# Kernel optimization log

Measured on AMD Instinct MI355X. Metric: run time of the kernel, lower is better.

## Reference

```python
import jax, jax.numpy as jnp
import numpy as np

EMBED_DIM = 1024
NUM_HEADS = 16
HEAD_DIM = EMBED_DIM // NUM_HEADS


def setup_inputs() -> dict:
    key = jax.random.key(0)
    k1, k2, k3, k4 = jax.random.split(key, 4)
    B, N, D = 4, 2048, EMBED_DIM
    x = jax.random.normal(k1, (B, N, D), dtype=jnp.float32)
    # torch nn.Linear layout: weight [out_features, in_features]
    w_qkv = jax.random.normal(k2, (3 * D, D), dtype=jnp.float32) * (1.0 / np.sqrt(D))
    w_out = jax.random.normal(k3, (D, D), dtype=jnp.float32) * (1.0 / np.sqrt(D))
    b_out = jax.random.normal(k4, (D,), dtype=jnp.float32) * 0.01
    return {"x": x, "w_qkv": w_qkv, "w_out": w_out, "b_out": b_out}


def reference(x, w_qkv, w_out, b_out):
    B, N, D = x.shape
    H, Hd = NUM_HEADS, HEAD_DIM
    qkv = (x @ w_qkv.T).reshape(B, N, 3, H, Hd)
    q, k, v = qkv[:, :, 0], qkv[:, :, 1], qkv[:, :, 2]  # [B,N,H,Hd]
    # NOTE: contracts over BOTH heads and head_dim -> single shared [B,N,N] map
    scores = jnp.einsum('bnhd,bmhd->bnm', q, k) / np.sqrt(Hd).astype(np.float32)
    attn = jax.nn.softmax(scores, axis=-1)
    out = jnp.einsum('bnm,bmhd->bnhd', attn, v).reshape(B, N, D)
    return out @ w_out.T + b_out
```

## Files before the change

kernel.cpp:

```cpp
#include <hip/hip_runtime.h>


typedef __bf16 bf16;
typedef __attribute__((ext_vector_type(8))) __bf16 bf16x8;
typedef __attribute__((ext_vector_type(4))) __bf16 bf16x4;
typedef __attribute__((ext_vector_type(16))) float f32x16;

#define BATCH 4
#define NTOK  2048
#define DIM   1024
#define MROWS (BATCH * NTOK)
#define QKVC  (3 * DIM)

__device__ __forceinline__ void async16(const bf16* g, bf16* l) {
  __builtin_amdgcn_global_load_lds(
      (const __attribute__((address_space(1))) void*)g,
      (__attribute__((address_space(3))) void*)l, 16, 0, 0);
}

__device__ __forceinline__ void cvt4(const float* in, bf16* out, int i4) {
  float4 f = *(const float4*)(in + i4 * 4);
  bf16x4 o;
  o.x = (bf16)f.x; o.y = (bf16)f.y; o.z = (bf16)f.z; o.w = (bf16)f.w;
  *(bf16x4*)(out + i4 * 4) = o;
}

__global__ void prep(const float* __restrict__ x, const float* __restrict__ wqkv,
                     const float* __restrict__ wout,
                     bf16* __restrict__ Xbf, bf16* __restrict__ Wqkvb,
                     bf16* __restrict__ Woutb, float* __restrict__ L) {
  const int nx = MROWS * DIM / 4, nq = QKVC * DIM / 4, nw = DIM * DIM / 4;
  const int nl = BATCH * NTOK / 4;
  int i = blockIdx.x * blockDim.x + threadIdx.x;
  if (i < nx) cvt4(x, Xbf, i);
  else if (i < nx + nq) cvt4(wqkv, Wqkvb, i - nx);
  else if (i < nx + nq + nw) cvt4(wout, Woutb, i - nx - nq);
  else if (i < nx + nq + nw + nl) {
    float4 z = {0.f, 0.f, 0.f, 0.f};
    *(float4*)(L + (i - nx - nq - nw) * 4) = z;
  }
}

struct GemmCore {
  const bf16 *ga[4], *gb[4];
  int sIdx[4];
  int wm, wn, l31, half;
};

__device__ __forceinline__ GemmCore gemm_setup(const bf16* A, const bf16* Bm,
                                               int lda, int ldb,
                                               long rowA, long rowB) {
  GemmCore g;
  const int tid = threadIdx.x;
  const int wave = tid >> 6, lane = tid & 63;
  g.wm = (wave >> 1) << 6;
  g.wn = (wave & 1) << 6;
  g.l31 = lane & 31;
  g.half = lane >> 5;
  const int srow = tid >> 3;
  const int sc   = tid & 7;
  const int scol = (sc ^ (srow & 7)) << 3;
#pragma unroll
  for (int seg = 0; seg < 4; ++seg) {
    g.ga[seg] = A  + (rowA + srow + 32 * seg) * (long)lda + scol;
    g.gb[seg] = Bm + (rowB + srow + 32 * seg) * (long)ldb + scol;
    g.sIdx[seg] = (srow + 32 * seg) * 64 + sc * 8;
  }
  return g;
}

__device__ __forceinline__ void gemm_kloop(const GemmCore& g, int K,
                                           bf16* As, bf16* Bs, f32x16 acc[2][2]) {
  const int sw = g.l31 & 7;
  for (int kt = 0; kt < K; kt += 64) {
#pragma unroll
    for (int seg = 0; seg < 4; ++seg) {
      async16(g.ga[seg] + kt, As + g.sIdx[seg]);
      async16(g.gb[seg] + kt, Bs + g.sIdx[seg]);
    }
    __syncthreads();

    bf16x8 af[2][4], bfm[2][4];
#pragma unroll
    for (int ti = 0; ti < 2; ++ti)
#pragma unroll
      for (int s = 0; s < 4; ++s)
        af[ti][s] = *(const bf16x8*)&As[(g.wm + ti * 32 + g.l31) * 64 + ((s * 2 + g.half) ^ sw) * 8];
#pragma unroll
    for (int tj = 0; tj < 2; ++tj)
#pragma unroll
      for (int s = 0; s < 4; ++s)
        bfm[tj][s] = *(const bf16x8*)&Bs[(g.wn + tj * 32 + g.l31) * 64 + ((s * 2 + g.half) ^ sw) * 8];

#pragma unroll
    for (int s = 0; s < 4; ++s)
#pragma unroll
      for (int ti = 0; ti < 2; ++ti)
#pragma unroll
        for (int tj = 0; tj < 2; ++tj)
          acc[ti][tj] = __builtin_amdgcn_mfma_f32_32x32x16_bf16(
              af[ti][s], bfm[tj][s], acc[ti][tj], 0, 0, 0);

    __syncthreads();
  }
}

template <int MODE>
__launch_bounds__(256)
__global__ void gemm_bt(const bf16* __restrict__ Aroot, const bf16* __restrict__ Broot,
                        void* __restrict__ Croot, const float* __restrict__ bias,
                        const float* __restrict__ Lroot,
                        int K, int lda, int ldb, int ldc,
                        long strideA, long strideB, long strideC) {
  const bf16* A  = Aroot + (long)blockIdx.z * strideA;
  const bf16* Bm = Broot + (long)blockIdx.z * strideB;
  __shared__ alignas(16) bf16 As[128 * 64];
  __shared__ alignas(16) bf16 Bs[128 * 64];

  const long rowA = (long)blockIdx.y * 128;
  const long rowB = (long)blockIdx.x * 128;
  GemmCore g = gemm_setup(A, Bm, lda, ldb, rowA, rowB);

  f32x16 acc[2][2] = {};
  gemm_kloop(g, K, As, Bs, acc);

  if constexpr (MODE == 0) {
    bf16* C = (bf16*)Croot + (long)blockIdx.z * strideC;
#pragma unroll
    for (int ti = 0; ti < 2; ++ti)
#pragma unroll
      for (int tj = 0; tj < 2; ++tj) {
        const long col = rowB + g.wn + tj * 32 + g.l31;
#pragma unroll
        for (int r = 0; r < 16; ++r) {
          const long row = rowA + g.wm + ti * 32 + (r & 3) + 8 * (r >> 2) + 4 * g.half;
          C[row * (long)ldc + col] = (bf16)acc[ti][tj][r];
        }
      }
  } else {
    float* C = (float*)Croot + (long)blockIdx.z * strideC;
    const float* L = Lroot + (long)blockIdx.z * NTOK;
#pragma unroll
    for (int ti = 0; ti < 2; ++ti) {
#pragma unroll
      for (int r = 0; r < 16; ++r) {
        const long row = rowA + g.wm + ti * 32 + (r & 3) + 8 * (r >> 2) + 4 * g.half;
        const float inv = 1.0f / L[row];
#pragma unroll
        for (int tj = 0; tj < 2; ++tj) {
          const long col = rowB + g.wn + tj * 32 + g.l31;
          C[row * (long)ldc + col] = acc[ti][tj][r] * inv + bias[col];
        }
      }
    }
  }
}

__launch_bounds__(256)
__global__ void gemm_sv(const bf16* __restrict__ QKV, const bf16* __restrict__ Wout,
                        bf16* __restrict__ E, bf16* __restrict__ Vpp,
                        float* __restrict__ Lroot) {
  __shared__ alignas(16) bf16 As[128 * 64];
  __shared__ alignas(16) bf16 Bs[128 * 64];

  const int z = blockIdx.z;
  if (z < 4) {
    const bf16* A  = QKV + (long)z * NTOK * QKVC;
    const bf16* Bm = A + DIM;
    const long rowA = (long)blockIdx.y * 128;
    const long rowB = (long)blockIdx.x * 128;
    GemmCore g = gemm_setup(A, Bm, QKVC, QKVC, rowA, rowB);
    f32x16 acc[2][2] = {};
    gemm_kloop(g, DIM, As, Bs, acc);

    bf16* C = E + (long)z * NTOK * NTOK;
    float* L = Lroot + (long)z * NTOK;
#pragma unroll
    for (int ti = 0; ti < 2; ++ti) {
#pragma unroll
      for (int r = 0; r < 16; ++r) {
        const long row = rowA + g.wm + ti * 32 + (r & 3) + 8 * (r >> 2) + 4 * g.half;
        float psum = 0.f;
#pragma unroll
        for (int tj = 0; tj < 2; ++tj) {
          const long col = rowB + g.wn + tj * 32 + g.l31;
          float e = __expf(acc[ti][tj][r] * 0.125f);
          bf16 eb = (bf16)e;
          C[row * (long)NTOK + col] = eb;
          psum += (float)eb;
        }
#pragma unroll
        for (int off = 16; off >= 1; off >>= 1) psum += __shfl_xor(psum, off, 64);
        if (g.l31 == 0) atomicAdd(&L[row], psum);
      }
    }
  } else {
    if (blockIdx.y >= 8) return;
    const int b = z - 4;
    const bf16* Bm = QKV + (long)b * NTOK * QKVC + 2 * DIM;
    const long rowA = (long)blockIdx.y * 128;
    const long rowB = (long)blockIdx.x * 128;
    GemmCore g = gemm_setup(Wout, Bm, DIM, QKVC, rowA, rowB);
    f32x16 acc[2][2] = {};
    gemm_kloop(g, DIM, As, Bs, acc);

    bf16* C = Vpp + (long)b * DIM * NTOK;
#pragma unroll
    for (int ti = 0; ti < 2; ++ti)
#pragma unroll
      for (int tj = 0; tj < 2; ++tj) {
        const long col = rowB + g.wn + tj * 32 + g.l31;
#pragma unroll
        for (int r = 0; r < 16; ++r) {
          const long row = rowA + g.wm + ti * 32 + (r & 3) + 8 * (r >> 2) + 4 * g.half;
          C[row * (long)NTOK + col] = (bf16)acc[ti][tj][r];
        }
      }
  }
}

extern "C" void kernel_launch(void* const* d_in, const int* in_sizes, int n_in,
                              void* d_out, int out_size, void* d_ws, size_t ws_size,
                              hipStream_t stream) {
  const float* x      = (const float*)d_in[0];
  const float* w_qkv  = (const float*)d_in[1];
  const float* w_out  = (const float*)d_in[2];
  const float* b_out  = (const float*)d_in[3];
  float* out = (float*)d_out;

  char* w = (char*)d_ws;
  bf16*  Xbf   = (bf16*)(w);
  bf16*  Wqkvb = (bf16*)(w + 16777216);
  bf16*  Woutb = (bf16*)(w + 23068672);
  bf16*  QKV   = (bf16*)(w + 25165824);
  bf16*  E     = (bf16*)(w + 75497472);
  bf16*  Vpp   = (bf16*)(w + 109051904);
  float* L     = (float*)(w + 125829120);

  {
    const int n4 = MROWS * DIM / 4 + QKVC * DIM / 4 + DIM * DIM / 4 + BATCH * NTOK / 4;
    prep<<<(n4 + 255) / 256, 256, 0, stream>>>(x, w_qkv, w_out, Xbf, Wqkvb, Woutb, L);
  }

  gemm_bt<0><<<dim3(QKVC / 128, MROWS / 128, 1), 256, 0, stream>>>(
      Xbf, Wqkvb, QKV, nullptr, nullptr, DIM, DIM, DIM, QKVC, 0, 0, 0);

  gemm_sv<<<dim3(NTOK / 128, NTOK / 128, 2 * BATCH), 256, 0, stream>>>(
      QKV, Woutb, E, Vpp, L);

  gemm_bt<2><<<dim3(DIM / 128, NTOK / 128, BATCH), 256, 0, stream>>>(
      E, Vpp, out, b_out, L, NTOK, NTOK, NTOK, DIM,
      (long)NTOK * NTOK, (long)DIM * NTOK, (long)NTOK * DIM);
}
```

Baseline: 271.1 us.

## Use 256x256 double-buffered pipelined GEMM for QKV and score/V' projections

Replaces the 128x128 single-buffered GEMM used for the QKV projection and the fused scores/Vout stage with a 256x256-tile, 512-thread kernel. It uses 128KB of dynamic LDS and double-buffers K-tiles so async global-to-LDS loads overlap the MFMA work, with fine-grained vmcnt waits, barriers and setprio. Larger tiles raise arithmetic intensity and cut global traffic. In exchange, fewer blocks give coarser occupancy and wave quantization, and the dynamic shared memory size may need an explicit attribute to launch.

```diff
diff --git a/kernel.cpp b/kernel.cpp
--- a/kernel.cpp
+++ b/kernel.cpp
@@ -11,6 +11,7 @@
 #define DIM   1024
 #define MROWS (BATCH * NTOK)
 #define QKVC  (3 * DIM)
+#define KT256 16
 
 __device__ __forceinline__ void async16(const bf16* g, bf16* l) {
   __builtin_amdgcn_global_load_lds(
@@ -41,6 +42,180 @@
   }
 }
 
+
+template <bool MORE>
+__device__ __forceinline__ void g256_iter(
+    const bf16* Ac, const bf16* Bc, bf16* An, bf16* Bn, int kn,
+    const bf16* gA0, const bf16* gA1, const bf16* gB0, const bf16* gB1,
+    int dst, const int rA[4], const int rB[2], int f, int half,
+    f32x16 acc[4][2]) {
+#pragma unroll
+  for (int p = 0; p < 4; ++p) {
+    const int c = (p & 1) * 2 + half;
+    const int co = ((c ^ f) & 3) * 8 + (p >> 1) * 8192;
+    bf16x8 av[4], bv[2];
+#pragma unroll
+    for (int ti = 0; ti < 4; ++ti) av[ti] = *(const bf16x8*)&Ac[rA[ti] + co];
+#pragma unroll
+    for (int tj = 0; tj < 2; ++tj) bv[tj] = *(const bf16x8*)&Bc[rB[tj] + co];
+    if (MORE) {
+      if (p == 0)      { async16(gA0 + kn,      An + dst);         async16(gA1 + kn,      An + 4096  + dst); }
+      else if (p == 1) { async16(gB0 + kn,      Bn + dst);         async16(gB1 + kn,      Bn + 4096  + dst); }
+      else if (p == 2) { async16(gA0 + kn + 32, An + 8192 + dst);  async16(gA1 + kn + 32, An + 12288 + dst); }
+      else             { async16(gB0 + kn + 32, Bn + 8192 + dst);  async16(gB1 + kn + 32, Bn + 12288 + dst); }
+    }
+    if (p & 1) {
+      if (MORE) asm volatile("s_waitcnt vmcnt(4)" ::: "memory");
+      else      asm volatile("s_waitcnt vmcnt(0)" ::: "memory");
+    }
+    __builtin_amdgcn_sched_barrier(0);
+    __builtin_amdgcn_s_barrier();
+    __builtin_amdgcn_sched_barrier(0);
+    asm volatile("s_waitcnt lgkmcnt(0)" ::: "memory");
+    __builtin_amdgcn_sched_barrier(0);
+    __builtin_amdgcn_s_setprio(1);
+#pragma unroll
+    for (int ti = 0; ti < 4; ++ti)
+#pragma unroll
+      for (int tj = 0; tj < 2; ++tj)
+        acc[ti][tj] = __builtin_amdgcn_mfma_f32_32x32x16_bf16(
+            av[ti], bv[tj], acc[ti][tj], 0, 0, 0);
+    __builtin_amdgcn_s_setprio(0);
+    __builtin_amdgcn_sched_barrier(0);
+    __builtin_amdgcn_s_barrier();
+    __builtin_amdgcn_sched_barrier(0);
+  }
+}
+
+__device__ __forceinline__ void gemm256(const bf16* __restrict__ A,
+                                        const bf16* __restrict__ Bm,
+                                        int lda, int ldb, long rowA, long rowB,
+                                        bf16* sm, int l31, int half, int wr, int wc,
+                                        f32x16 acc[4][2]) {
+  const int tid = threadIdx.x;
+  const int sr = tid >> 2, sq = tid & 3;
+  const int sf = (sr >> 1) & 3;
+  const int scol = (sq ^ sf) * 8;
+  const bf16* gA0 = A  + (rowA + sr) * (long)lda + scol;
+  const bf16* gA1 = A  + (rowA + sr + 128) * (long)lda + scol;
+  const bf16* gB0 = Bm + (rowB + sr) * (long)ldb + scol;
+  const bf16* gB1 = Bm + (rowB + sr + 128) * (long)ldb + scol;
+
+  bf16* Ab0 = sm;
+  bf16* Ab1 = sm + 16384;
+  bf16* Bb0 = sm + 32768;
+  bf16* Bb1 = sm + 49152;
+  const int dst = tid * 8;
+
+  int rA[4], rB[2];
+#pragma unroll
+  for (int ti = 0; ti < 4; ++ti) rA[ti] = (wr * 128 + ti * 32 + l31) * 32;
+#pragma unroll
+  for (int tj = 0; tj < 2; ++tj) rB[tj] = (wc * 64 + tj * 32 + l31) * 32;
+  const int f = (l31 >> 1) & 3;
+
+  async16(gA0, Ab0 + dst);            async16(gA1, Ab0 + 4096 + dst);
+  async16(gB0, Bb0 + dst);            async16(gB1, Bb0 + 4096 + dst);
+  async16(gA0 + 32, Ab0 + 8192 + dst); async16(gA1 + 32, Ab0 + 12288 + dst);
+  async16(gB0 + 32, Bb0 + 8192 + dst); async16(gB1 + 32, Bb0 + 12288 + dst);
+  asm volatile("s_waitcnt vmcnt(4)" ::: "memory");
+  __builtin_amdgcn_sched_barrier(0);
+  __builtin_amdgcn_s_barrier();
+  __builtin_amdgcn_sched_barrier(0);
+
+#pragma unroll 1
+  for (int t2 = 0; t2 < 7; ++t2) {
+    g256_iter<true >(Ab0, Bb0, Ab1, Bb1, (2 * t2 + 1) * 64, gA0, gA1, gB0, gB1, dst, rA, rB, f, half, acc);
+    g256_iter<true >(Ab1, Bb1, Ab0, Bb0, (2 * t2 + 2) * 64, gA0, gA1, gB0, gB1, dst, rA, rB, f, half, acc);
+  }
+  g256_iter<true >(Ab0, Bb0, Ab1, Bb1, 15 * 64, gA0, gA1, gB0, gB1, dst, rA, rB, f, half, acc);
+  g256_iter<false>(Ab1, Bb1, Ab0, Bb0, 0,       gA0, gA1, gB0, gB1, dst, rA, rB, f, half, acc);
+}
+
+__launch_bounds__(512, 2)
+__global__ void gemm256_qkv(const bf16* __restrict__ Xb, const bf16* __restrict__ Wq,
+                            bf16* __restrict__ QKV) {
+  extern __shared__ bf16 sm[];
+  const int tid = threadIdx.x, wave = tid >> 6, lane = tid & 63;
+  const int wr = wave >> 2, wc = wave & 3, l31 = lane & 31, half = lane >> 5;
+  const long rowA = (long)blockIdx.y * 256;
+  const long rowB = (long)blockIdx.x * 256;
+  f32x16 acc[4][2] = {};
+  gemm256(Xb, Wq, DIM, DIM, rowA, rowB, sm, l31, half, wr, wc, acc);
+#pragma unroll
+  for (int ti = 0; ti < 4; ++ti)
+#pragma unroll
+    for (int tj = 0; tj < 2; ++tj) {
+      const long col = rowB + wc * 64 + tj * 32 + l31;
+#pragma unroll
+      for (int r = 0; r < 16; ++r) {
+        const long row = rowA + wr * 128 + ti * 32 + (r & 3) + 8 * (r >> 2) + 4 * half;
+        QKV[row * (long)QKVC + col] = (bf16)acc[ti][tj][r];
+      }
+    }
+}
+
+__launch_bounds__(512, 2)
+__global__ void gemm256_sv(const bf16* __restrict__ QKV, const bf16* __restrict__ Wout,
+                           bf16* __restrict__ E, bf16* __restrict__ Vpp,
+                           float* __restrict__ Lroot) {
+  extern __shared__ bf16 sm[];
+  const int tid = threadIdx.x, wave = tid >> 6, lane = tid & 63;
+  const int wr = wave >> 2, wc = wave & 3, l31 = lane & 31, half = lane >> 5;
+  const int z = blockIdx.z;
+  if (z < 4) {
+    const bf16* A  = QKV + (long)z * NTOK * QKVC;
+    const bf16* Bm = A + DIM;
+    const long rowA = (long)blockIdx.y * 256;
+    const long rowB = (long)blockIdx.x * 256;
+    f32x16 acc[4][2] = {};
+    gemm256(A, Bm, QKVC, QKVC, rowA, rowB, sm, l31, half, wr, wc, acc);
+
+    bf16* C = E + (long)z * NTOK * NTOK;
+    float* L = Lroot + (long)z * NTOK;
+#pragma unroll
+    for (int ti = 0; ti < 4; ++ti) {
+#pragma unroll
+      for (int r = 0; r < 16; ++r) {
+        const long row = rowA + wr * 128 + ti * 32 + (r & 3) + 8 * (r >> 2) + 4 * half;
+        float psum = 0.f;
+#pragma unroll
+        for (int tj = 0; tj < 2; ++tj) {
+          const long col = rowB + wc * 64 + tj * 32 + l31;
+          float e = __expf(acc[ti][tj][r] * 0.125f);
+          bf16 eb = (bf16)e;
+          C[row * (long)NTOK + col] = eb;
+          psum += (float)eb;
+        }
+#pragma unroll
+        for (int off = 16; off >= 1; off >>= 1) psum += __shfl_xor(psum, off, 64);
+        if (l31 == 0) atomicAdd(&L[row], psum);
+      }
+    }
+  } else {
+    if (blockIdx.y >= 4) return;
+    const int b = z - 4;
+    const bf16* Bm = QKV + (long)b * NTOK * QKVC + 2 * DIM;
+    const long rowA = (long)blockIdx.y * 256;
+    const long rowB = (long)blockIdx.x * 256;
+    f32x16 acc[4][2] = {};
+    gemm256(Wout, Bm, DIM, QKVC, rowA, rowB, sm, l31, half, wr, wc, acc);
+
+    bf16* C = Vpp + (long)b * DIM * NTOK;
+#pragma unroll
+    for (int ti = 0; ti < 4; ++ti)
+#pragma unroll
+      for (int tj = 0; tj < 2; ++tj) {
+        const long col = rowB + wc * 64 + tj * 32 + l31;
+#pragma unroll
+        for (int r = 0; r < 16; ++r) {
+          const long row = rowA + wr * 128 + ti * 32 + (r & 3) + 8 * (r >> 2) + 4 * half;
+          C[row * (long)NTOK + col] = (bf16)acc[ti][tj][r];
+        }
+      }
+  }
+}
+
 struct GemmCore {
   const bf16 *ga[4], *gb[4];
   int sIdx[4];
@@ -156,69 +331,6 @@
   }
 }
 
-__launch_bounds__(256)
-__global__ void gemm_sv(const bf16* __restrict__ QKV, const bf16* __restrict__ Wout,
-                        bf16* __restrict__ E, bf16* __restrict__ Vpp,
-                        float* __restrict__ Lroot) {
-  __shared__ alignas(16) bf16 As[128 * 64];
-  __shared__ alignas(16) bf16 Bs[128 * 64];
-
-  const int z = blockIdx.z;
-  if (z < 4) {
-    const bf16* A  = QKV + (long)z * NTOK * QKVC;
-    const bf16* Bm = A + DIM;
-    const long rowA = (long)blockIdx.y * 128;
-    const long rowB = (long)blockIdx.x * 128;
-    GemmCore g = gemm_setup(A, Bm, QKVC, QKVC, rowA, rowB);
-    f32x16 acc[2][2] = {};
-    gemm_kloop(g, DIM, As, Bs, acc);
-
-    bf16* C = E + (long)z * NTOK * NTOK;
-    float* L = Lroot + (long)z * NTOK;
-#pragma unroll
-    for (int ti = 0; ti < 2; ++ti) {
-#pragma unroll
-      for (int r = 0; r < 16; ++r) {
-        const long row = rowA + g.wm + ti * 32 + (r & 3) + 8 * (r >> 2) + 4 * g.half;
-        float psum = 0.f;
-#pragma unroll
-        for (int tj = 0; tj < 2; ++tj) {
-          const long col = rowB + g.wn + tj * 32 + g.l31;
-          float e = __expf(acc[ti][tj][r] * 0.125f);
-          bf16 eb = (bf16)e;
-          C[row * (long)NTOK + col] = eb;
-          psum += (float)eb;
-        }
-#pragma unroll
-        for (int off = 16; off >= 1; off >>= 1) psum += __shfl_xor(psum, off, 64);
-        if (g.l31 == 0) atomicAdd(&L[row], psum);
-      }
-    }
-  } else {
-    if (blockIdx.y >= 8) return;
-    const int b = z - 4;
-    const bf16* Bm = QKV + (long)b * NTOK * QKVC + 2 * DIM;
-    const long rowA = (long)blockIdx.y * 128;
-    const long rowB = (long)blockIdx.x * 128;
-    GemmCore g = gemm_setup(Wout, Bm, DIM, QKVC, rowA, rowB);
-    f32x16 acc[2][2] = {};
-    gemm_kloop(g, DIM, As, Bs, acc);
-
-    bf16* C = Vpp + (long)b * DIM * NTOK;
-#pragma unroll
-    for (int ti = 0; ti < 2; ++ti)
-#pragma unroll
-      for (int tj = 0; tj < 2; ++tj) {
-        const long col = rowB + g.wn + tj * 32 + g.l31;
-#pragma unroll
-        for (int r = 0; r < 16; ++r) {
-          const long row = rowA + g.wm + ti * 32 + (r & 3) + 8 * (r >> 2) + 4 * g.half;
-          C[row * (long)NTOK + col] = (bf16)acc[ti][tj][r];
-        }
-      }
-  }
-}
-
 extern "C" void kernel_launch(void* const* d_in, const int* in_sizes, int n_in,
                               void* d_out, int out_size, void* d_ws, size_t ws_size,
                               hipStream_t stream) {
@@ -242,10 +354,10 @@
     prep<<<(n4 + 255) / 256, 256, 0, stream>>>(x, w_qkv, w_out, Xbf, Wqkvb, Woutb, L);
   }
 
-  gemm_bt<0><<<dim3(QKVC / 128, MROWS / 128, 1), 256, 0, stream>>>(
-      Xbf, Wqkvb, QKV, nullptr, nullptr, DIM, DIM, DIM, QKVC, 0, 0, 0);
-
-  gemm_sv<<<dim3(NTOK / 128, NTOK / 128, 2 * BATCH), 256, 0, stream>>>(
+  gemm256_qkv<<<dim3(QKVC / 256, MROWS / 256, 1), 512, 131072, stream>>>(
+      Xbf, Wqkvb, QKV);
+
+  gemm256_sv<<<dim3(NTOK / 256, NTOK / 256, 2 * BATCH), 512, 131072, stream>>>(
       QKV, Woutb, E, Vpp, L);
 
   gemm_bt<2><<<dim3(DIM / 128, NTOK / 128, BATCH), 256, 0, stream>>>(
```

New measurement: 281.8 us. 1.04x slower.

## Double-buffer LDS tiles to overlap global loads with MFMA compute

Applied to the files above, without the earlier changes.

Replaces the single-buffer load/sync/compute/sync GEMM loop with a ping-pong pair of LDS buffers, so the next K tile is fetched asynchronously while the current one is computed. This leaves one barrier per tile instead of two. LDS use doubles to 64 KB per block, which may lower occupancy. The loop assumes K/64 is even and at least 2, which holds for all call sites.

```diff
diff --git a/kernel.cpp b/kernel.cpp
--- a/kernel.cpp
+++ b/kernel.cpp
@@ -69,40 +69,66 @@
   return g;
 }
 
+__device__ __forceinline__ void stage_tile(const GemmCore& g, int kt,
+                                           bf16* As, bf16* Bs) {
+#pragma unroll
+  for (int seg = 0; seg < 4; ++seg) {
+    async16(g.ga[seg] + kt, As + g.sIdx[seg]);
+    async16(g.gb[seg] + kt, Bs + g.sIdx[seg]);
+  }
+}
+
+__device__ __forceinline__ void compute_tile(const GemmCore& g,
+                                             const bf16* As, const bf16* Bs,
+                                             f32x16 acc[2][2]) {
+  const int sw = g.l31 & 7;
+  bf16x8 af[2][4], bfm[2][4];
+#pragma unroll
+  for (int ti = 0; ti < 2; ++ti)
+#pragma unroll
+    for (int s = 0; s < 4; ++s)
+      af[ti][s] = *(const bf16x8*)&As[(g.wm + ti * 32 + g.l31) * 64 + ((s * 2 + g.half) ^ sw) * 8];
+#pragma unroll
+  for (int tj = 0; tj < 2; ++tj)
+#pragma unroll
+    for (int s = 0; s < 4; ++s)
+      bfm[tj][s] = *(const bf16x8*)&Bs[(g.wn + tj * 32 + g.l31) * 64 + ((s * 2 + g.half) ^ sw) * 8];
+
+#pragma unroll
+  for (int s = 0; s < 4; ++s)
+#pragma unroll
+    for (int ti = 0; ti < 2; ++ti)
+#pragma unroll
+      for (int tj = 0; tj < 2; ++tj)
+        acc[ti][tj] = __builtin_amdgcn_mfma_f32_32x32x16_bf16(
+            af[ti][s], bfm[tj][s], acc[ti][tj], 0, 0, 0);
+}
+
+__device__ __forceinline__ void sync_tile() {
+  asm volatile("s_waitcnt vmcnt(0) lgkmcnt(0)" ::: "memory");
+  __builtin_amdgcn_s_barrier();
+}
+
 __device__ __forceinline__ void gemm_kloop(const GemmCore& g, int K,
-                                           bf16* As, bf16* Bs, f32x16 acc[2][2]) {
-  const int sw = g.l31 & 7;
-  for (int kt = 0; kt < K; kt += 64) {
-#pragma unroll
-    for (int seg = 0; seg < 4; ++seg) {
-      async16(g.ga[seg] + kt, As + g.sIdx[seg]);
-      async16(g.gb[seg] + kt, Bs + g.sIdx[seg]);
-    }
-    __syncthreads();
-
-    bf16x8 af[2][4], bfm[2][4];
-#pragma unroll
-    for (int ti = 0; ti < 2; ++ti)
-#pragma unroll
-      for (int s = 0; s < 4; ++s)
-        af[ti][s] = *(const bf16x8*)&As[(g.wm + ti * 32 + g.l31) * 64 + ((s * 2 + g.half) ^ sw) * 8];
-#pragma unroll
-    for (int tj = 0; tj < 2; ++tj)
-#pragma unroll
-      for (int s = 0; s < 4; ++s)
-        bfm[tj][s] = *(const bf16x8*)&Bs[(g.wn + tj * 32 + g.l31) * 64 + ((s * 2 + g.half) ^ sw) * 8];
-
-#pragma unroll
-    for (int s = 0; s < 4; ++s)
-#pragma unroll
-      for (int ti = 0; ti < 2; ++ti)
-#pragma unroll
-        for (int tj = 0; tj < 2; ++tj)
-          acc[ti][tj] = __builtin_amdgcn_mfma_f32_32x32x16_bf16(
-              af[ti][s], bfm[tj][s], acc[ti][tj], 0, 0, 0);
-
-    __syncthreads();
-  }
+                                           bf16* As0, bf16* Bs0,
+                                           bf16* As1, bf16* Bs1,
+                                           f32x16 acc[2][2]) {
+  stage_tile(g, 0, As0, Bs0);
+  sync_tile();
+  const int nt = K >> 6;
+#pragma unroll 1
+  for (int t2 = 0; t2 < nt / 2 - 1; ++t2) {
+    stage_tile(g, (2 * t2 + 1) * 64, As1, Bs1);
+    compute_tile(g, As0, Bs0, acc);
+    sync_tile();
+    stage_tile(g, (2 * t2 + 2) * 64, As0, Bs0);
+    compute_tile(g, As1, Bs1, acc);
+    sync_tile();
+  }
+  stage_tile(g, (nt - 1) * 64, As1, Bs1);
+  compute_tile(g, As0, Bs0, acc);
+  sync_tile();
+  compute_tile(g, As1, Bs1, acc);
 }
 
 template <int MODE>
@@ -114,15 +140,17 @@
                         long strideA, long strideB, long strideC) {
   const bf16* A  = Aroot + (long)blockIdx.z * strideA;
   const bf16* Bm = Broot + (long)blockIdx.z * strideB;
-  __shared__ alignas(16) bf16 As[128 * 64];
-  __shared__ alignas(16) bf16 Bs[128 * 64];
+  __shared__ alignas(16) bf16 As0[128 * 64];
+  __shared__ alignas(16) bf16 Bs0[128 * 64];
+  __shared__ alignas(16) bf16 As1[128 * 64];
+  __shared__ alignas(16) bf16 Bs1[128 * 64];
 
   const long rowA = (long)blockIdx.y * 128;
   const long rowB = (long)blockIdx.x * 128;
   GemmCore g = gemm_setup(A, Bm, lda, ldb, rowA, rowB);
 
   f32x16 acc[2][2] = {};
-  gemm_kloop(g, K, As, Bs, acc);
+  gemm_kloop(g, K, As0, Bs0, As1, Bs1, acc);
 
   if constexpr (MODE == 0) {
     bf16* C = (bf16*)Croot + (long)blockIdx.z * strideC;
@@ -160,8 +188,10 @@
 __global__ void gemm_sv(const bf16* __restrict__ QKV, const bf16* __restrict__ Wout,
                         bf16* __restrict__ E, bf16* __restrict__ Vpp,
                         float* __restrict__ Lroot) {
-  __shared__ alignas(16) bf16 As[128 * 64];
-  __shared__ alignas(16) bf16 Bs[128 * 64];
+  __shared__ alignas(16) bf16 As0[128 * 64];
+  __shared__ alignas(16) bf16 Bs0[128 * 64];
+  __shared__ alignas(16) bf16 As1[128 * 64];
+  __shared__ alignas(16) bf16 Bs1[128 * 64];
 
   const int z = blockIdx.z;
   if (z < 4) {
@@ -171,7 +201,7 @@
     const long rowB = (long)blockIdx.x * 128;
     GemmCore g = gemm_setup(A, Bm, QKVC, QKVC, rowA, rowB);
     f32x16 acc[2][2] = {};
-    gemm_kloop(g, DIM, As, Bs, acc);
+    gemm_kloop(g, DIM, As0, Bs0, As1, Bs1, acc);
 
     bf16* C = E + (long)z * NTOK * NTOK;
     float* L = Lroot + (long)z * NTOK;
@@ -202,7 +232,7 @@
     const long rowB = (long)blockIdx.x * 128;
     GemmCore g = gemm_setup(Wout, Bm, DIM, QKVC, rowA, rowB);
     f32x16 acc[2][2] = {};
-    gemm_kloop(g, DIM, As, Bs, acc);
+    gemm_kloop(g, DIM, As0, Bs0, As1, Bs1, acc);
 
     bf16* C = Vpp + (long)b * DIM * NTOK;
 #pragma unroll
```

Measured after the change: 267.3 us. About the same (-1.4%).
